# Kernel tuning notes

Measured on AMD Instinct MI355X. Metric: run time of the kernel, lower is better.

Reference implementation:

```python
import jax, jax.numpy as jnp
import numpy as np

N_NODES = 100_000
N_EDGES = 1_600_000
D_IN = 128
D_HID = 128
D_OUT = 128
N_GRAPHS = 1024


def setup_inputs() -> dict:
    key = jax.random.key(0)
    ks = jax.random.split(key, 7)
    x = jax.random.normal(ks[0], (N_NODES, D_IN), dtype=jnp.float32)
    edge_index = jax.random.randint(ks[1], (2, N_EDGES), 0, N_NODES, dtype=jnp.int32)
    batch = jnp.sort(jax.random.randint(ks[2], (N_NODES,), 0, N_GRAPHS, dtype=jnp.int32))
    W1 = jax.random.normal(ks[3], (D_IN, D_HID), dtype=jnp.float32) * (1.0 / np.sqrt(D_IN))
    b1 = jax.random.normal(ks[4], (D_HID,), dtype=jnp.float32) * 0.01
    W2 = jax.random.normal(ks[5], (D_HID, D_OUT), dtype=jnp.float32) * (1.0 / np.sqrt(D_HID))
    b2 = jax.random.normal(ks[6], (D_OUT,), dtype=jnp.float32) * 0.01
    return {"x": x, "edge_index": edge_index, "batch": batch,
            "W1": W1, "b1": b1, "W2": W2, "b2": b2, "num_graphs": N_GRAPHS}


def gcn_conv(x, edge_index, W, b):
    """PyG GCNConv: add self-loops, symmetric deg^{-1/2} norm, linear, scatter-add."""
    n = x.shape[0]
    xw = x @ W  # [N, H] -- transform before propagate, as PyG does
    loop = jnp.arange(n, dtype=edge_index.dtype)
    src = jnp.concatenate([edge_index[0], loop])  # message source (x_j)
    dst = jnp.concatenate([edge_index[1], loop])  # aggregation target
    deg = jax.ops.segment_sum(jnp.ones_like(dst, dtype=xw.dtype), dst, num_segments=n)
    dinv = jnp.where(deg > 0, jax.lax.rsqrt(deg), 0.0)
    norm = dinv[src] * dinv[dst]  # [E+N]
    out = jax.ops.segment_sum(norm[:, None] * xw[src], dst, num_segments=n)
    return out + b


def reference(x, edge_index, batch, W1, b1, W2, b2, num_graphs):
    h = jax.nn.relu(gcn_conv(x, edge_index, W1, b1))
    h = gcn_conv(h, edge_index, W2, b2)
    # global_mean_pool over graph ids
    s = jax.ops.segment_sum(h, batch, num_segments=num_graphs)          # [G, D_OUT]
    cnt = jax.ops.segment_sum(jnp.ones((x.shape[0],), h.dtype), batch, num_segments=num_graphs)
    return s / jnp.maximum(cnt, 1.0)[:, None]
```

## Files before the change

kernel.cpp:

```cpp
#include <hip/hip_runtime.h>

constexpr int D = 128;
constexpr int PAD = 48;
constexpr int EBLK = 4096;
constexpr int WNODE = 256;
constexpr int CAPW = 32;
constexpr int SCAP = 8192;

typedef __attribute__((ext_vector_type(8))) short short8;
typedef __attribute__((ext_vector_type(4))) float floatx4;
typedef __attribute__((ext_vector_type(2))) float floatx2;
typedef unsigned short ushort_t;
typedef unsigned char uchar_t;

static inline size_t ws_align(size_t x) { return (x + 255) & ~size_t(255); }

__device__ inline unsigned pack_bf16(float a, float b) {
  unsigned ua = __float_as_uint(a), ub = __float_as_uint(b);
  ua += 0x7fffu + ((ua >> 16) & 1u);
  ub += 0x7fffu + ((ub >> 16) & 1u);
  return ((ua >> 16) & 0xffffu) | (ub & 0xffff0000u);
}
__device__ inline ushort_t f32_to_bf16u(float f) {
  unsigned u = __float_as_uint(f);
  u += 0x7fffu + ((u >> 16) & 1u);
  return (ushort_t)(u >> 16);
}
__device__ inline float bf16u_to_f32(ushort_t u) {
  return __uint_as_float(((unsigned)u) << 16);
}
__device__ inline uchar_t f32_to_fp8(float v) {
  int p = __builtin_amdgcn_cvt_pk_fp8_f32(v, v, 0, false);
  return (uchar_t)(p & 0xff);
}
__device__ inline void fp8x4_acc(unsigned u, float* v) {
  floatx2 a = __builtin_amdgcn_cvt_pk_f32_fp8((int)u, false);
  floatx2 b = __builtin_amdgcn_cvt_pk_f32_fp8((int)u, true);
  v[0] += a.x; v[1] += a.y; v[2] += b.x; v[3] += b.y;
}
__device__ inline void fp8x4_acc2(unsigned u, floatx2* v) {
  v[0] += __builtin_amdgcn_cvt_pk_f32_fp8((int)u, false);
  v[1] += __builtin_amdgcn_cvt_pk_f32_fp8((int)u, true);
}

__global__ __launch_bounds__(256) void k_prep(
    const int* __restrict__ src, const int* __restrict__ dst, int E,
    int nstrips, int nw,
    unsigned* __restrict__ bucket, int* __restrict__ bkcnt,
    uint2* __restrict__ spill, int* __restrict__ scnt,
    const float* __restrict__ W1, const float* __restrict__ W2,
    ushort_t* __restrict__ w1t, ushort_t* __restrict__ w2t, int nbin) {
  const int b = blockIdx.x;
  const int t = threadIdx.x;
  if (b < nbin) {
    __shared__ int lcnt[512];
    for (int i = t; i < nw; i += 256) lcnt[i] = 0;
    __syncthreads();
    const int base = b * EBLK;
    const int end = min(base + EBLK, E);
    for (int j = base + t; j < end; j += 256) {
      int ss = src[j], dd = dst[j];
      int wnd = dd >> 8;
      unsigned pk = ((unsigned)(dd & 255) << 17) | (unsigned)ss;
      int p = atomicAdd(&lcnt[wnd], 1);
      if (p < CAPW) {
        bucket[((size_t)wnd * nstrips + b) * CAPW + p] = pk;
      } else {
        int sp = atomicAdd(scnt, 1);
        if (sp < SCAP) spill[sp] = make_uint2((unsigned)ss, (unsigned)dd);
      }
    }
    __syncthreads();
    for (int i = t; i < nw; i += 256)
      bkcnt[(size_t)i * nstrips + b] = min(lcnt[i], CAPW);
    return;
  }
  {
    int idx = (b - nbin) * 256 + t;
    int k = idx >> 7, n = idx & 127;
    w1t[n * 128 + k] = f32_to_bf16u(W1[idx]);
    w2t[n * 128 + k] = f32_to_bf16u(W2[idx]);
  }
}

__global__ __launch_bounds__(256) void k_fill(
    const unsigned* __restrict__ bucket, const int* __restrict__ bkcnt,
    const uint2* __restrict__ spill, const int* __restrict__ scnt,
    int* __restrict__ cnt, int* __restrict__ csrp, int N, int nstrips) {
  __shared__ int lc[WNODE];
  __shared__ int ls[WNODE * PAD];
  const int w = blockIdx.x;
  const int t = threadIdx.x;
  const int wbase = w << 8;
  const int nn = min(WNODE, N - wbase);
  for (int i = t; i < WNODE; i += 256) lc[i] = 0;
  __syncthreads();
  const int* bc = bkcnt + (size_t)w * nstrips;
  const unsigned* bwin = bucket + (size_t)w * nstrips * CAPW;
  const int wid = t >> 6, l = t & 63;
  const int sgrp = l >> 3;
  const int ui = l & 7;
  for (int sb0 = wid * 8; sb0 < nstrips; sb0 += 32) {
    int s = sb0 + sgrp;
    int c = (s < nstrips) ? bc[s] : 0;
    uint4 v = make_uint4(0u, 0u, 0u, 0u);
    if (ui * 4 < c)
      v = ((const uint4*)(bwin + (size_t)s * CAPW))[ui];
    unsigned e[4] = {v.x, v.y, v.z, v.w};
#pragma unroll
    for (int u = 0; u < 4; ++u) {
      int j = ui * 4 + u;
      if (j < c) {
        unsigned pk = e[u];
        int dl = (int)(pk >> 17);
        int p = atomicAdd(&lc[dl], 1);
        if (p < PAD) ls[dl * PAD + p] = (int)(pk & 0x1FFFFu);
      }
    }
  }
  {
    int ns = min(*scnt, SCAP);
    for (int j = t; j < ns; j += 256) {
      uint2 e = spill[j];
      if ((int)(e.y >> 8) == w) {
        int dl = (int)(e.y & 255u);
        int p = atomicAdd(&lc[dl], 1);
        if (p < PAD) ls[dl * PAD + p] = (int)e.x;
      }
    }
  }
  __syncthreads();
  const int total = nn * PAD;
  int4* dp = (int4*)(csrp + (size_t)wbase * PAD);
  const int4* sp = (const int4*)ls;
  for (int i = t; i < (total >> 2); i += 256) dp[i] = sp[i];
  for (int i = (total & ~3) + t; i < total; i += 256)
    csrp[(size_t)wbase * PAD + i] = ls[i];
  for (int i = t; i < nn; i += 256) cnt[wbase + i] = lc[i];
}

template <bool A_FP32>
__global__ __launch_bounds__(512) void k_gemm(
    const void* __restrict__ Av, const ushort_t* __restrict__ Wt,
    const int* __restrict__ cnt, uchar_t* __restrict__ Y, int N) {
  __shared__ ushort_t As[64 * 128];
  __shared__ ushort_t Bs[128 * 128];
  const int t = threadIdx.x;
  const int rowBase = blockIdx.x * 64;

  {
    const uint4* g = (const uint4*)Wt;
#pragma unroll
    for (int i = 0; i < 4; ++i) {
      int idx = t + 512 * i;
      int r = idx >> 4, c = idx & 15;
      int cs = c ^ (r & 15);
      *(uint4*)&Bs[r * 128 + cs * 8] = g[idx];
    }
  }
  if (A_FP32) {
    const float4* A = (const float4*)Av;
#pragma unroll
    for (int i = 0; i < 4; ++i) {
      int idx = t + 512 * i;
      int r = idx >> 5, c4 = idx & 31;
      int grow = rowBase + r;
      float4 v = make_float4(0.f, 0.f, 0.f, 0.f);
      if (grow < N) v = A[(size_t)grow * 32 + c4];
      int cs = (c4 >> 1) ^ (r & 15);
      unsigned* p = (unsigned*)&As[r * 128 + cs * 8 + (c4 & 1) * 4];
      p[0] = pack_bf16(v.x, v.y);
      p[1] = pack_bf16(v.z, v.w);
    }
  } else {
    const uint4* A = (const uint4*)Av;
#pragma unroll
    for (int i = 0; i < 2; ++i) {
      int idx = t + 512 * i;
      int r = idx >> 4, c = idx & 15;
      int grow = rowBase + r;
      uint4 v = make_uint4(0u, 0u, 0u, 0u);
      if (grow < N) v = A[(size_t)grow * 16 + c];
      int cs = c ^ (r & 15);
      *(uint4*)&As[r * 128 + cs * 8] = v;
    }
  }
  __syncthreads();

  const int w = t >> 6;
  const int l = t & 63;
  const int qd = l >> 4, lm = l & 15;
  const int mrow = (w >> 1) * 16;
  const int jb = (w & 1) * 4;

  floatx4 acc[4];
#pragma unroll
  for (int j = 0; j < 4; ++j) acc[j] = (floatx4){0.f, 0.f, 0.f, 0.f};

#pragma unroll
  for (int ks = 0; ks < 4; ++ks) {
    const int ch = ks * 4 + qd;
    const int chs = ch ^ lm;
    short8 a0 = *(const short8*)&As[(mrow + lm) * 128 + chs * 8];
#pragma unroll
    for (int j = 0; j < 4; ++j) {
      short8 b = *(const short8*)&Bs[((jb + j) * 16 + lm) * 128 + chs * 8];
      acc[j] = __builtin_amdgcn_mfma_f32_16x16x32_bf16(a0, b, acc[j], 0, 0, 0);
    }
  }

  float s[4];
#pragma unroll
  for (int r = 0; r < 4; ++r) {
    int grow = rowBase + mrow + qd * 4 + r;
    s[r] = (grow < N) ? rsqrtf(1.f + (float)cnt[grow]) : 0.f;
  }
#pragma unroll
  for (int j = 0; j < 4; ++j)
#pragma unroll
    for (int r = 0; r < 4; ++r) {
      int grow = rowBase + mrow + qd * 4 + r;
      if (grow < N)
        Y[(size_t)grow * 128 + (jb + j) * 16 + lm] = f32_to_fp8(s[r] * acc[j][r]);
    }
}

template <bool RELU>
__global__ __launch_bounds__(256) void k_aggregate(
    const uchar_t* __restrict__ y, const int* __restrict__ csrp,
    const int* __restrict__ cnt, const float* __restrict__ bias,
    ushort_t* __restrict__ out, int N) {
  const int wid = threadIdx.x >> 6;
  const int n0 = blockIdx.x * 8 + wid * 2;
  if (n0 >= N) return;
  const int n1 = n0 + 1;
  const bool hasB = (n1 < N);
  const int l = threadIdx.x & 63;
  const int eg = l >> 4, q = l & 15;
  const uint2* yb = (const uint2*)y;
  int degA0 = cnt[n0];
  int degB0 = hasB ? cnt[n1] : 0;
  float dvA = rsqrtf(1.f + (float)degA0);
  float dvB = rsqrtf(1.f + (float)degB0);
  int degA = degA0 > PAD ? PAD : degA0;
  int degB = degB0 > PAD ? PAD : degB0;
  int idxA = 0, idxB = 0;
  if (l < PAD) {
    idxA = csrp[(size_t)n0 * PAD + l];
    if (hasB) idxB = csrp[(size_t)n1 * PAD + l];
  }
  uint2 sv = make_uint2(0u, 0u);
  if (eg == 0) sv = yb[(size_t)n0 * 16 + q];
  else if (eg == 1 && hasB) sv = yb[(size_t)n1 * 16 + q];
  floatx2 vA[4], vB[4];
#pragma unroll
  for (int k = 0; k < 4; ++k) { vA[k] = (floatx2){0.f, 0.f}; vB[k] = (floatx2){0.f, 0.f}; }
  const int dmax = degA > degB ? degA : degB;
  const int iters = (dmax + 15) >> 4;
  for (int it = 0; it < iters; ++it) {
    int p0 = it * 16 + eg;
    int p1 = p0 + 4, p2 = p0 + 8, p3 = p0 + 12;
    int a0 = __shfl(idxA, p0);
    int a1 = __shfl(idxA, p1);
    int a2 = __shfl(idxA, p2);
    int a3 = __shfl(idxA, p3);
    int b0 = __shfl(idxB, p0);
    int b1 = __shfl(idxB, p1);
    int b2 = __shfl(idxB, p2);
    int b3 = __shfl(idxB, p3);
    if (p0 < degA) { uint2 v = yb[(size_t)a0 * 16 + q]; fp8x4_acc2(v.x, vA); fp8x4_acc2(v.y, vA + 2); }
    if (p0 < degB) { uint2 v = yb[(size_t)b0 * 16 + q]; fp8x4_acc2(v.x, vB); fp8x4_acc2(v.y, vB + 2); }
    if (p1 < degA) { uint2 v = yb[(size_t)a1 * 16 + q]; fp8x4_acc2(v.x, vA); fp8x4_acc2(v.y, vA + 2); }
    if (p1 < degB) { uint2 v = yb[(size_t)b1 * 16 + q]; fp8x4_acc2(v.x, vB); fp8x4_acc2(v.y, vB + 2); }
    if (p2 < degA) { uint2 v = yb[(size_t)a2 * 16 + q]; fp8x4_acc2(v.x, vA); fp8x4_acc2(v.y, vA + 2); }
    if (p2 < degB) { uint2 v = yb[(size_t)b2 * 16 + q]; fp8x4_acc2(v.x, vB); fp8x4_acc2(v.y, vB + 2); }
    if (p3 < degA) { uint2 v = yb[(size_t)a3 * 16 + q]; fp8x4_acc2(v.x, vA); fp8x4_acc2(v.y, vA + 2); }
    if (p3 < degB) { uint2 v = yb[(size_t)b3 * 16 + q]; fp8x4_acc2(v.x, vB); fp8x4_acc2(v.y, vB + 2); }
  }
  float fA[8] = {vA[0].x, vA[0].y, vA[1].x, vA[1].y, vA[2].x, vA[2].y, vA[3].x, vA[3].y};
  float fB[8] = {vB[0].x, vB[0].y, vB[1].x, vB[1].y, vB[2].x, vB[2].y, vB[3].x, vB[3].y};
#pragma unroll
  for (int k = 0; k < 8; ++k) {
    fA[k] += __shfl_xor(fA[k], 32); fA[k] += __shfl_xor(fA[k], 16);
    fB[k] += __shfl_xor(fB[k], 32); fB[k] += __shfl_xor(fB[k], 16);
  }
  if (eg == 0 || (eg == 1 && hasB)) {
    float dv = (eg == 0) ? dvA : dvB;
    int node = (eg == 0) ? n0 : n1;
    float f[8];
#pragma unroll
    for (int k = 0; k < 8; ++k) f[k] = (eg == 0) ? fA[k] : fB[k];
    fp8x4_acc(sv.x, f); fp8x4_acc(sv.y, f + 4);
    float4 c0 = ((const float4*)bias)[2 * q];
    float4 c1 = ((const float4*)bias)[2 * q + 1];
    float o[8];
    o[0] = dv * f[0] + c0.x; o[1] = dv * f[1] + c0.y;
    o[2] = dv * f[2] + c0.z; o[3] = dv * f[3] + c0.w;
    o[4] = dv * f[4] + c1.x; o[5] = dv * f[5] + c1.y;
    o[6] = dv * f[6] + c1.z; o[7] = dv * f[7] + c1.w;
    if (RELU) {
#pragma unroll
      for (int k = 0; k < 8; ++k) o[k] = fmaxf(o[k], 0.f);
    }
    uint4 pk;
    pk.x = pack_bf16(o[0], o[1]); pk.y = pack_bf16(o[2], o[3]);
    pk.z = pack_bf16(o[4], o[5]); pk.w = pack_bf16(o[6], o[7]);
    ((uint4*)out)[(size_t)node * 16 + q] = pk;
  }
}

__global__ __launch_bounds__(512) void k_pool(
    const ushort_t* __restrict__ h, const int* __restrict__ batch,
    float* __restrict__ out, int N, int G) {
  __shared__ float part[4][128];
  int g = blockIdx.x;
  int col = threadIdx.x & 127;
  int pr = threadIdx.x >> 7;
  int lo = 0, hi = N;
  while (lo < hi) { int m = (lo + hi) >> 1; if (batch[m] < g) lo = m + 1; else hi = m; }
  int start = lo;
  hi = N;
  while (lo < hi) { int m = (lo + hi) >> 1; if (batch[m] <= g) lo = m + 1; else hi = m; }
  int end = lo;
  float sum = 0.f;
  for (int r = start + pr; r < end; r += 4) sum += bf16u_to_f32(h[(size_t)r * D + col]);
  part[pr][col] = sum;
  __syncthreads();
  if (pr == 0) {
    float s = part[0][col] + part[1][col] + part[2][col] + part[3][col];
    int c = end - start;
    out[(size_t)g * D + col] = s / (float)(c > 0 ? c : 1);
  }
}

extern "C" void kernel_launch(void* const* d_in, const int* in_sizes, int n_in,
                              void* d_out, int out_size, void* d_ws, size_t ws_size,
                              hipStream_t stream) {
  const float* x  = (const float*)d_in[0];
  const int* edge = (const int*)d_in[1];
  const int* batch = (const int*)d_in[2];
  const float* W1 = (const float*)d_in[3];
  const float* b1 = (const float*)d_in[4];
  const float* W2 = (const float*)d_in[5];
  const float* b2 = (const float*)d_in[6];
  float* out = (float*)d_out;

  const int N = in_sizes[0] / D;
  const int E = in_sizes[1] / 2;
  const int G = out_size / D;
  const int* esrc = edge;
  const int* edst = edge + E;

  const int nstrips = (E + EBLK - 1) / EBLK;
  const int nw = (N + WNODE - 1) / WNODE;

  char* ws = (char*)d_ws;
  size_t off = 0;
  auto alloc = [&](size_t bytes) {
    char* p = ws + off;
    off = ws_align(off + bytes);
    return p;
  };
  uchar_t* bufY = (uchar_t*)alloc((size_t)N * D);
  ushort_t* bufH = (ushort_t*)alloc((size_t)N * D * 2);
  int* cnt = (int*)alloc((size_t)N * 4);
  int* csrp = (int*)alloc((size_t)N * PAD * 4);
  ushort_t* w1t = (ushort_t*)alloc((size_t)D * D * 2);
  ushort_t* w2t = (ushort_t*)alloc((size_t)D * D * 2);
  unsigned* bucket = (unsigned*)alloc((size_t)nw * nstrips * CAPW * 4);
  int* bkcnt = (int*)alloc((size_t)nw * nstrips * 4);
  uint2* spill = (uint2*)alloc((size_t)SCAP * 8);
  int* scnt = (int*)alloc(256);

  const int tb = 256;

  hipMemsetAsync(scnt, 0, 4, stream);

  const int nbin = nstrips;
  const int nwp = (D * D) / 256;
  k_prep<<<nbin + nwp, tb, 0, stream>>>(esrc, edst, E, nstrips, nw,
                                        bucket, bkcnt, spill, scnt,
                                        W1, W2, w1t, w2t, nbin);

  k_fill<<<nw, tb, 0, stream>>>(bucket, bkcnt, spill, scnt, cnt, csrp, N, nstrips);

  const int gblk = (N + 63) / 64;
  const int ablk = (N + 7) / 8;
  k_gemm<true><<<gblk, 512, 0, stream>>>(x, w1t, cnt, bufY, N);
  k_aggregate<true><<<ablk, 256, 0, stream>>>(bufY, csrp, cnt, b1, bufH, N);
  k_gemm<false><<<gblk, 512, 0, stream>>>(bufH, w2t, cnt, bufY, N);
  k_aggregate<false><<<ablk, 256, 0, stream>>>(bufY, csrp, cnt, b2, bufH, N);
  k_pool<<<G, 512, 0, stream>>>(bufH, batch, out, N, G);
}
```

Before: 267.1 us.

## Fuse layer-1 aggregation with layer-2 GEMM into one kernel

Adds a kernel in which each 512-thread block aggregates neighbour features for 16 nodes, applies bias and ReLU, stores the bf16 rows in shared memory, and multiplies them by W2 with MFMA to produce the scaled fp8 layer-2 input directly. This removes one launch and the round trip of the bf16 hidden activations through global memory. The cost is that every block reloads the full 128x128 W2 tile into 32KB of LDS for only 16 rows, which adds load traffic and may limit occupancy. A second fp8 buffer is added so the kernel does not overwrite its own input.

Result: no change. 264.7 us (median of 2 runs) (-0.9%).

```diff
diff --git a/kernel.cpp b/kernel.cpp
--- a/kernel.cpp
+++ b/kernel.cpp
@@ -225,6 +225,125 @@
     }
 }
 
+__global__ __launch_bounds__(512) void k_agg_gemm(
+    const uchar_t* __restrict__ y, const int* __restrict__ csrp,
+    const int* __restrict__ cnt, const float* __restrict__ bias,
+    const ushort_t* __restrict__ Wt, uchar_t* __restrict__ Y2, int N) {
+  __shared__ ushort_t Hs[16 * 128];
+  __shared__ ushort_t Bs[128 * 128];
+  const int t = threadIdx.x;
+  const int wid = t >> 6;
+  const int l = t & 63;
+  const int eg = l >> 4, q = l & 15;
+  const int base = blockIdx.x * 16;
+  {
+    const uint4* g = (const uint4*)Wt;
+#pragma unroll
+    for (int i = 0; i < 4; ++i) {
+      int idx = t + 512 * i;
+      int r = idx >> 4, c = idx & 15;
+      int cs = c ^ (r & 15);
+      *(uint4*)&Bs[r * 128 + cs * 8] = g[idx];
+    }
+  }
+  const int n0 = base + wid * 2;
+  if (n0 < N) {
+    const int n1 = n0 + 1;
+    const bool hasB = (n1 < N);
+    const uint2* yb = (const uint2*)y;
+    int degA0 = cnt[n0];
+    int degB0 = hasB ? cnt[n1] : 0;
+    float dvA = rsqrtf(1.f + (float)degA0);
+    float dvB = rsqrtf(1.f + (float)degB0);
+    int degA = degA0 > PAD ? PAD : degA0;
+    int degB = degB0 > PAD ? PAD : degB0;
+    int idxA = 0, idxB = 0;
+    if (l < PAD) {
+      idxA = csrp[(size_t)n0 * PAD + l];
+      if (hasB) idxB = csrp[(size_t)n1 * PAD + l];
+    }
+    uint2 sv = make_uint2(0u, 0u);
+    if (eg == 0) sv = yb[(size_t)n0 * 16 + q];
+    else if (eg == 1 && hasB) sv = yb[(size_t)n1 * 16 + q];
+    floatx2 vA[4], vB[4];
+#pragma unroll
+    for (int k = 0; k < 4; ++k) { vA[k] = (floatx2){0.f, 0.f}; vB[k] = (floatx2){0.f, 0.f}; }
+    const int dmax = degA > degB ? degA : degB;
+    const int iters = (dmax + 15) >> 4;
+    for (int it = 0; it < iters; ++it) {
+      int p0 = it * 16 + eg;
+      int p1 = p0 + 4, p2 = p0 + 8, p3 = p0 + 12;
+      int a0 = __shfl(idxA, p0);
+      int a1 = __shfl(idxA, p1);
+      int a2 = __shfl(idxA, p2);
+      int a3 = __shfl(idxA, p3);
+      int b0 = __shfl(idxB, p0);
+      int b1 = __shfl(idxB, p1);
+      int b2 = __shfl(idxB, p2);
+      int b3 = __shfl(idxB, p3);
+      if (p0 < degA) { uint2 v = yb[(size_t)a0 * 16 + q]; fp8x4_acc2(v.x, vA); fp8x4_acc2(v.y, vA + 2); }
+      if (p0 < degB) { uint2 v = yb[(size_t)b0 * 16 + q]; fp8x4_acc2(v.x, vB); fp8x4_acc2(v.y, vB + 2); }
+      if (p1 < degA) { uint2 v = yb[(size_t)a1 * 16 + q]; fp8x4_acc2(v.x, vA); fp8x4_acc2(v.y, vA + 2); }
+      if (p1 < degB) { uint2 v = yb[(size_t)b1 * 16 + q]; fp8x4_acc2(v.x, vB); fp8x4_acc2(v.y, vB + 2); }
+      if (p2 < degA) { uint2 v = yb[(size_t)a2 * 16 + q]; fp8x4_acc2(v.x, vA); fp8x4_acc2(v.y, vA + 2); }
+      if (p2 < degB) { uint2 v = yb[(size_t)b2 * 16 + q]; fp8x4_acc2(v.x, vB); fp8x4_acc2(v.y, vB + 2); }
+      if (p3 < degA) { uint2 v = yb[(size_t)a3 * 16 + q]; fp8x4_acc2(v.x, vA); fp8x4_acc2(v.y, vA + 2); }
+      if (p3 < degB) { uint2 v = yb[(size_t)b3 * 16 + q]; fp8x4_acc2(v.x, vB); fp8x4_acc2(v.y, vB + 2); }
+    }
+    float fA[8] = {vA[0].x, vA[0].y, vA[1].x, vA[1].y, vA[2].x, vA[2].y, vA[3].x, vA[3].y};
+    float fB[8] = {vB[0].x, vB[0].y, vB[1].x, vB[1].y, vB[2].x, vB[2].y, vB[3].x, vB[3].y};
+#pragma unroll
+    for (int k = 0; k < 8; ++k) {
+      fA[k] += __shfl_xor(fA[k], 32); fA[k] += __shfl_xor(fA[k], 16);
+      fB[k] += __shfl_xor(fB[k], 32); fB[k] += __shfl_xor(fB[k], 16);
+    }
+    if (eg == 0 || (eg == 1 && hasB)) {
+      float dv = (eg == 0) ? dvA : dvB;
+      float f[8];
+#pragma unroll
+      for (int k = 0; k < 8; ++k) f[k] = (eg == 0) ? fA[k] : fB[k];
+      fp8x4_acc(sv.x, f); fp8x4_acc(sv.y, f + 4);
+      float4 c0 = ((const float4*)bias)[2 * q];
+      float4 c1 = ((const float4*)bias)[2 * q + 1];
+      float o[8];
+      o[0] = dv * f[0] + c0.x; o[1] = dv * f[1] + c0.y;
+      o[2] = dv * f[2] + c0.z; o[3] = dv * f[3] + c0.w;
+      o[4] = dv * f[4] + c1.x; o[5] = dv * f[5] + c1.y;
+      o[6] = dv * f[6] + c1.z; o[7] = dv * f[7] + c1.w;
+#pragma unroll
+      for (int k = 0; k < 8; ++k) o[k] = fmaxf(o[k], 0.f);
+      uint4 pk;
+      pk.x = pack_bf16(o[0], o[1]); pk.y = pack_bf16(o[2], o[3]);
+      pk.z = pack_bf16(o[4], o[5]); pk.w = pack_bf16(o[6], o[7]);
+      int r = wid * 2 + eg;
+      int cs = q ^ r;
+      *(uint4*)&Hs[r * 128 + cs * 8] = pk;
+    }
+  }
+  __syncthreads();
+  floatx4 acc = (floatx4){0.f, 0.f, 0.f, 0.f};
+#pragma unroll
+  for (int ks = 0; ks < 4; ++ks) {
+    const int ch = ks * 4 + eg;
+    const int chs = ch ^ q;
+    short8 a0 = *(const short8*)&Hs[q * 128 + chs * 8];
+    short8 b = *(const short8*)&Bs[(wid * 16 + q) * 128 + chs * 8];
+    acc = __builtin_amdgcn_mfma_f32_16x16x32_bf16(a0, b, acc, 0, 0, 0);
+  }
+  float s[4];
+#pragma unroll
+  for (int r = 0; r < 4; ++r) {
+    int grow = base + eg * 4 + r;
+    s[r] = (grow < N) ? rsqrtf(1.f + (float)cnt[grow]) : 0.f;
+  }
+#pragma unroll
+  for (int r = 0; r < 4; ++r) {
+    int grow = base + eg * 4 + r;
+    if (grow < N)
+      Y2[(size_t)grow * 128 + wid * 16 + q] = f32_to_fp8(s[r] * acc[r]);
+  }
+}
+
 template <bool RELU>
 __global__ __launch_bounds__(256) void k_aggregate(
     const uchar_t* __restrict__ y, const int* __restrict__ csrp,
@@ -362,6 +481,7 @@
     return p;
   };
   uchar_t* bufY = (uchar_t*)alloc((size_t)N * D);
+  uchar_t* bufY2 = (uchar_t*)alloc((size_t)N * D);
   ushort_t* bufH = (ushort_t*)alloc((size_t)N * D * 2);
   int* cnt = (int*)alloc((size_t)N * 4);
   int* csrp = (int*)alloc((size_t)N * PAD * 4);
@@ -385,10 +505,10 @@
   k_fill<<<nw, tb, 0, stream>>>(bucket, bkcnt, spill, scnt, cnt, csrp, N, nstrips);
 
   const int gblk = (N + 63) / 64;
+  k_gemm<true><<<gblk, 512, 0, stream>>>(x, w1t, cnt, bufY, N);
+  const int fblk = (N + 15) / 16;
+  k_agg_gemm<<<fblk, 512, 0, stream>>>(bufY, csrp, cnt, b1, w2t, bufY2, N);
   const int ablk = (N + 7) / 8;
-  k_gemm<true><<<gblk, 512, 0, stream>>>(x, w1t, cnt, bufY, N);
-  k_aggregate<true><<<ablk, 256, 0, stream>>>(bufY, csrp, cnt, b1, bufH, N);
-  k_gemm<false><<<gblk, 512, 0, stream>>>(bufH, w2t, cnt, bufY, N);
-  k_aggregate<false><<<ablk, 256, 0, stream>>>(bufY, csrp, cnt, b2, bufH, N);
+  k_aggregate<false><<<ablk, 256, 0, stream>>>(bufY2, csrp, cnt, b2, bufH, N);
   k_pool<<<G, 512, 0, stream>>>(bufH, batch, out, N, G);
 }
```
